# Optimization experiments

Hardware: AMD Instinct MI355X
Metric: run time of the kernel (lower is better)

Reference implementation:

```python
import jax, jax.numpy as jnp
import numpy as np

N_NODES = 100000
IN_CH = 256
HIDDEN = 256
N_EDGES = 500000


def setup_inputs() -> dict:
    key = jax.random.key(0)
    k_emb, k_ei, k_w1, k_w2 = jax.random.split(key, 4)
    embeddings = jax.random.normal(k_emb, (N_NODES, IN_CH), dtype=jnp.float32)
    edge_index = jax.random.randint(k_ei, (2, N_EDGES), 0, N_NODES, dtype=jnp.int64)
    # Linear(in*2, hidden) and Linear(hidden, 1) weights (stored input-major for x @ W)
    s1 = 1.0 / np.sqrt(2 * IN_CH)
    s2 = 1.0 / np.sqrt(HIDDEN)
    W1 = jax.random.uniform(k_w1, (2 * IN_CH, HIDDEN), dtype=jnp.float32, minval=-s1, maxval=s1)
    b1 = jnp.zeros((HIDDEN,), dtype=jnp.float32)
    W2 = jax.random.uniform(k_w2, (HIDDEN, 1), dtype=jnp.float32, minval=-s2, maxval=s2)
    b2 = jnp.zeros((1,), dtype=jnp.float32)
    return {"embeddings": embeddings, "edge_index": edge_index,
            "W1": W1, "b1": b1, "W2": W2, "b2": b2}


def reference(embeddings, edge_index, W1, b1, W2, b2):
    src, dst = edge_index[0], edge_index[1]
    # gather [E, in] twice, concat -> [E, 2*in]
    feats = jnp.concatenate([embeddings[src], embeddings[dst]], axis=-1)
    h = jax.nn.relu(feats @ W1 + b1)          # [E, hidden]
    scores = h @ W2 + b2                      # [E, 1]
    return scores.reshape(-1)
```

## Files before the change

### kernel.cpp

```cpp
#include <hip/hip_runtime.h>

#define NN   100000
#define EE   500000
#define MPAD 100096

using bf16x8 = __attribute__((ext_vector_type(8))) short;
using f32x4  = __attribute__((ext_vector_type(4))) float;
using u16x8  = __attribute__((ext_vector_type(8))) unsigned short;

__device__ __forceinline__ unsigned short f2bf(float f) {
  unsigned int x = __builtin_bit_cast(unsigned int, f);
  x += 0x7fffu + ((x >> 16) & 1u);
  return (unsigned short)(x >> 16);
}
__device__ __forceinline__ float bf2f(unsigned short u) {
  unsigned int x = ((unsigned int)u) << 16;
  return __builtin_bit_cast(float, x);
}

__global__ void wprep_kernel(const float* __restrict__ W1, unsigned short* __restrict__ WT) {
  int id = blockIdx.x * blockDim.x + threadIdx.x;
  if (id >= 512 * 32) return;
  int j  = id >> 5;
  int cg = id & 31;
  int jc = j & 255;
  int kb = (cg << 3) + ((j >= 256) ? 256 : 0);
  u16x8 v;
#pragma unroll
  for (int t = 0; t < 8; ++t)
    v[t] = f2bf(W1[(size_t)(kb + t) * 256 + jc]);
  *reinterpret_cast<u16x8*>(WT + (size_t)j * 256 + (cg << 3)) = v;
}

__global__ __launch_bounds__(512) void gemm_pq(const float* __restrict__ emb,
                                               const unsigned short* __restrict__ WT,
                                               const float* __restrict__ b1,
                                               unsigned short* __restrict__ R) {
  __shared__ unsigned short ldsA[2][128 * 32];
  __shared__ unsigned short ldsB[2][256 * 32];

  const int t    = threadIdx.x;
  const int lane = t & 63;
  const int wave = t >> 6;
  const int wrow = wave >> 2;
  const int wcol = wave & 3;
  const int m0   = (int)(blockIdx.x >> 1) * 128;
  const int n0   = (int)(blockIdx.x & 1) * 256;

  const int arow = t >> 2, ac = t & 3;
  const bool aOk = (m0 + arow) < NN;
  const float* aSrc = emb + (size_t)(m0 + arow) * 256 + (ac << 3);
  const int aW = arow * 32 + ((ac ^ ((arow >> 1) & 3)) << 3);

  const int brow = t >> 1, bh = t & 1;
  const unsigned short* bSrc = WT + (size_t)(n0 + brow) * 256 + (bh << 4);
  const int f_b = (brow >> 1) & 3;
  const int bW0 = brow * 32 + ((((bh << 1) | 0) ^ f_b) << 3);
  const int bW1 = brow * 32 + ((((bh << 1) | 1) ^ f_b) << 3);

  const int fr = lane & 15, fq = lane >> 4;
  int aoff[4], boff[4];
#pragma unroll
  for (int m = 0; m < 4; ++m) {
    int r = wrow * 64 + 16 * m + fr;
    aoff[m] = r * 32 + ((fq ^ ((r >> 1) & 3)) << 3);
  }
#pragma unroll
  for (int n = 0; n < 4; ++n) {
    int r = wcol * 64 + 16 * n + fr;
    boff[n] = r * 32 + ((fq ^ ((r >> 1) & 3)) << 3);
  }

  f32x4 acc[4][4] = {};

  {
    float4 a0, a1;
    if (aOk) { a0 = *(const float4*)aSrc; a1 = *(const float4*)(aSrc + 4); }
    else     { a0 = make_float4(0.f, 0.f, 0.f, 0.f); a1 = a0; }
    u16x8 b0 = *(const u16x8*)bSrc;
    u16x8 b1v = *(const u16x8*)(bSrc + 8);
    u16x8 aw;
    aw[0] = f2bf(a0.x); aw[1] = f2bf(a0.y); aw[2] = f2bf(a0.z); aw[3] = f2bf(a0.w);
    aw[4] = f2bf(a1.x); aw[5] = f2bf(a1.y); aw[6] = f2bf(a1.z); aw[7] = f2bf(a1.w);
    *(u16x8*)&ldsA[0][aW]  = aw;
    *(u16x8*)&ldsB[0][bW0] = b0;
    *(u16x8*)&ldsB[0][bW1] = b1v;
  }
  __syncthreads();

#pragma unroll
  for (int ks = 0; ks < 8; ++ks) {
    const int p = ks & 1;
    float4 na0, na1; u16x8 nb0, nb1;
    if (ks < 7) {
      const float* as = aSrc + ((ks + 1) << 5);
      if (aOk) { na0 = *(const float4*)as; na1 = *(const float4*)(as + 4); }
      else     { na0 = make_float4(0.f, 0.f, 0.f, 0.f); na1 = na0; }
      const unsigned short* bs = bSrc + ((ks + 1) << 5);
      nb0 = *(const u16x8*)bs;
      nb1 = *(const u16x8*)(bs + 8);
    }
    bf16x8 av[4], bv[4];
#pragma unroll
    for (int m = 0; m < 4; ++m) av[m] = *(const bf16x8*)&ldsA[p][aoff[m]];
#pragma unroll
    for (int n = 0; n < 4; ++n) bv[n] = *(const bf16x8*)&ldsB[p][boff[n]];
#pragma unroll
    for (int m = 0; m < 4; ++m)
#pragma unroll
      for (int n = 0; n < 4; ++n)
        acc[m][n] = __builtin_amdgcn_mfma_f32_16x16x32_bf16(av[m], bv[n], acc[m][n], 0, 0, 0);
    if (ks < 7) {
      u16x8 aw;
      aw[0] = f2bf(na0.x); aw[1] = f2bf(na0.y); aw[2] = f2bf(na0.z); aw[3] = f2bf(na0.w);
      aw[4] = f2bf(na1.x); aw[5] = f2bf(na1.y); aw[6] = f2bf(na1.z); aw[7] = f2bf(na1.w);
      *(u16x8*)&ldsA[p ^ 1][aW]  = aw;
      *(u16x8*)&ldsB[p ^ 1][bW0] = nb0;
      *(u16x8*)&ldsB[p ^ 1][bW1] = nb1;
    }
    __syncthreads();
  }

  float bn[4];
#pragma unroll
  for (int n = 0; n < 4; ++n) {
    const int c = n0 + wcol * 64 + 16 * n + fr;
    bn[n] = (c < 256) ? b1[c] : 0.f;
  }
#pragma unroll
  for (int m = 0; m < 4; ++m) {
    const int r0 = m0 + wrow * 64 + 16 * m + (fq << 2);
#pragma unroll
    for (int n = 0; n < 4; ++n) {
      const int c = n0 + wcol * 64 + 16 * n + fr;
#pragma unroll
      for (int i = 0; i < 4; ++i)
        R[(size_t)(r0 + i) * 512 + c] = f2bf(acc[m][n][i] + bn[n]);
    }
  }
}

__global__ __launch_bounds__(256) void edge_kernel(const int* __restrict__ idx,
                                                   const unsigned short* __restrict__ R,
                                                   const float* __restrict__ W2,
                                                   const float* __restrict__ b2,
                                                   float* __restrict__ out) {
  const int lane  = threadIdx.x & 63;
  const int half  = lane >> 5;
  const int l     = lane & 31;
  const int gwave = (int)((blockIdx.x * blockDim.x + threadIdx.x) >> 6);
  const int nwave = (int)((gridDim.x * blockDim.x) >> 6);
  const float4 w0 = *(const float4*)(W2 + (l << 3));
  const float4 w1 = *(const float4*)(W2 + (l << 3) + 4);
  const float bias = b2[0];

  for (int c = gwave; c < (EE / 8); c += nwave) {
    const int e0 = c << 3;
    int s[4], d[4];
#pragma unroll
    for (int u = 0; u < 4; ++u) {
      s[u] = idx[e0 + (u << 1) + half];
      d[u] = idx[EE + e0 + (u << 1) + half];
    }
    u16x8 ga[4], gb[4];
#pragma unroll
    for (int u = 0; u < 4; ++u) {
      ga[u] = *(const u16x8*)(R + (size_t)s[u] * 512 + (l << 3));
      gb[u] = *(const u16x8*)(R + (size_t)d[u] * 512 + 256 + (l << 3));
    }
#pragma unroll
    for (int u = 0; u < 4; ++u) {
      float acc;
      acc  = fmaxf(bf2f((unsigned short)ga[u][0]) + bf2f((unsigned short)gb[u][0]), 0.f) * w0.x;
      acc += fmaxf(bf2f((unsigned short)ga[u][1]) + bf2f((unsigned short)gb[u][1]), 0.f) * w0.y;
      acc += fmaxf(bf2f((unsigned short)ga[u][2]) + bf2f((unsigned short)gb[u][2]), 0.f) * w0.z;
      acc += fmaxf(bf2f((unsigned short)ga[u][3]) + bf2f((unsigned short)gb[u][3]), 0.f) * w0.w;
      acc += fmaxf(bf2f((unsigned short)ga[u][4]) + bf2f((unsigned short)gb[u][4]), 0.f) * w1.x;
      acc += fmaxf(bf2f((unsigned short)ga[u][5]) + bf2f((unsigned short)gb[u][5]), 0.f) * w1.y;
      acc += fmaxf(bf2f((unsigned short)ga[u][6]) + bf2f((unsigned short)gb[u][6]), 0.f) * w1.z;
      acc += fmaxf(bf2f((unsigned short)ga[u][7]) + bf2f((unsigned short)gb[u][7]), 0.f) * w1.w;
#pragma unroll
      for (int off = 16; off > 0; off >>= 1) acc += __shfl_xor(acc, off, 64);
      if (l == 0) out[e0 + (u << 1) + half] = acc + bias;
    }
  }
}

__global__ __launch_bounds__(256) void fallback_kernel(const float* __restrict__ emb,
                                                       const int* __restrict__ idx,
                                                       const float* __restrict__ W1,
                                                       const float* __restrict__ b1,
                                                       const float* __restrict__ W2,
                                                       const float* __restrict__ b2,
                                                       float* __restrict__ out) {
  __shared__ float feats[512];
  __shared__ float red[256];
  const int t = threadIdx.x;
  for (int e = blockIdx.x; e < EE; e += gridDim.x) {
    __syncthreads();
    const int s = idx[e], d = idx[EE + e];
    feats[t]       = emb[(size_t)s * 256 + t];
    feats[256 + t] = emb[(size_t)d * 256 + t];
    __syncthreads();
    float h = b1[t];
    for (int k = 0; k < 512; ++k) h += feats[k] * W1[k * 256 + t];
    red[t] = fmaxf(h, 0.f) * W2[t];
    __syncthreads();
    for (int off = 128; off > 0; off >>= 1) {
      if (t < off) red[t] += red[t + off];
      __syncthreads();
    }
    if (t == 0) out[e] = red[0] + b2[0];
  }
}

extern "C" void kernel_launch(void* const* d_in, const int* in_sizes, int n_in,
                              void* d_out, int out_size, void* d_ws, size_t ws_size,
                              hipStream_t stream) {
  const float* emb = (const float*)d_in[0];
  const int*   idx = (const int*)d_in[1];
  const float* W1  = (const float*)d_in[2];
  const float* b1  = (const float*)d_in[3];
  const float* W2  = (const float*)d_in[4];
  const float* b2  = (const float*)d_in[5];
  float* out = (float*)d_out;

  const size_t wt_elems = (size_t)512 * 256;
  const size_t r_elems  = (size_t)MPAD * 512;
  const size_t need = (wt_elems + r_elems) * sizeof(unsigned short);

  if (ws_size < need) {
    fallback_kernel<<<4096, 256, 0, stream>>>(emb, idx, W1, b1, W2, b2, out);
    return;
  }

  unsigned short* WT = (unsigned short*)d_ws;
  unsigned short* R  = WT + wt_elems;

  wprep_kernel<<<64, 256, 0, stream>>>(W1, WT);
  gemm_pq<<<782 * 2, 512, 0, stream>>>(emb, WT, b1, R);
  edge_kernel<<<2048, 256, 0, stream>>>(idx, R, W2, b2, out);
}
```

Before: 151.8 us.

## Shrink GEMM tile to 64 rows and read W1 fragments directly from global

The node-projection GEMM now uses 64-row tiles with 256-thread blocks, giving twice as many blocks. B fragments are loaded straight from global/L2 into registers instead of being staged through LDS. The K loop goes from 8 steps of 32 to 4 steps of 64 with double-buffered A, which halves the number of barriers. In exchange, B gets less reuse and global loads sit on the MFMA critical path, since B is not prefetched.

```diff
diff --git a/kernel.cpp b/kernel.cpp
--- a/kernel.cpp
+++ b/kernel.cpp
@@ -32,112 +32,116 @@
   *reinterpret_cast<u16x8*>(WT + (size_t)j * 256 + (cg << 3)) = v;
 }
 
-__global__ __launch_bounds__(512) void gemm_pq(const float* __restrict__ emb,
+__global__ __launch_bounds__(256) void gemm_pq(const float* __restrict__ emb,
                                                const unsigned short* __restrict__ WT,
                                                const float* __restrict__ b1,
                                                unsigned short* __restrict__ R) {
-  __shared__ unsigned short ldsA[2][128 * 32];
-  __shared__ unsigned short ldsB[2][256 * 32];
+  __shared__ unsigned short ldsA[2][2][64 * 32];
 
   const int t    = threadIdx.x;
   const int lane = t & 63;
   const int wave = t >> 6;
-  const int wrow = wave >> 2;
-  const int wcol = wave & 3;
-  const int m0   = (int)(blockIdx.x >> 1) * 128;
+  const int m0   = (int)(blockIdx.x >> 1) * 64;
   const int n0   = (int)(blockIdx.x & 1) * 256;
 
-  const int arow = t >> 2, ac = t & 3;
-  const bool aOk = (m0 + arow) < NN;
-  const float* aSrc = emb + (size_t)(m0 + arow) * 256 + (ac << 3);
-  const int aW = arow * 32 + ((ac ^ ((arow >> 1) & 3)) << 3);
-
-  const int brow = t >> 1, bh = t & 1;
-  const unsigned short* bSrc = WT + (size_t)(n0 + brow) * 256 + (bh << 4);
-  const int f_b = (brow >> 1) & 3;
-  const int bW0 = brow * 32 + ((((bh << 1) | 0) ^ f_b) << 3);
-  const int bW1 = brow * 32 + ((((bh << 1) | 1) ^ f_b) << 3);
+  const int a_r = t >> 2, a_j = t & 3;
+  const bool aOk = (m0 + a_r) < NN;
+  const float* aSrc = emb + (size_t)(m0 + a_r) * 256 + (a_j << 4);
+  const int a_s  = a_j >> 1;
+  const int fA   = (a_r >> 1) & 3;
+  const int aW0  = a_r * 32 + ((((a_j & 1) << 1) | 0) ^ fA) * 8;
+  const int aW1  = a_r * 32 + ((((a_j & 1) << 1) | 1) ^ fA) * 8;
 
   const int fr = lane & 15, fq = lane >> 4;
-  int aoff[4], boff[4];
+  const int fS = (fr >> 1) & 3;
+  int aoff[4];
+#pragma unroll
+  for (int m = 0; m < 4; ++m)
+    aoff[m] = (16 * m + fr) * 32 + ((fq ^ fS) << 3);
+
+  const unsigned short* bRow[4];
+#pragma unroll
+  for (int n = 0; n < 4; ++n)
+    bRow[n] = WT + (size_t)(n0 + wave * 64 + 16 * n + fr) * 256 + (fq << 3);
+
+  f32x4 acc[4][4] = {};
+  float4 pA[4];
+
+#define LOADA(kb)                                                              \
+  do {                                                                         \
+    if (aOk) {                                                                 \
+      pA[0] = *(const float4*)(aSrc + (kb));                                   \
+      pA[1] = *(const float4*)(aSrc + (kb) + 4);                               \
+      pA[2] = *(const float4*)(aSrc + (kb) + 8);                               \
+      pA[3] = *(const float4*)(aSrc + (kb) + 12);                              \
+    } else {                                                                   \
+      pA[0] = pA[1] = pA[2] = pA[3] = make_float4(0.f, 0.f, 0.f, 0.f);         \
+    }                                                                          \
+  } while (0)
+
+#define WRITEA(buf)                                                            \
+  do {                                                                         \
+    u16x8 w0, w1;                                                              \
+    w0[0] = f2bf(pA[0].x); w0[1] = f2bf(pA[0].y);                              \
+    w0[2] = f2bf(pA[0].z); w0[3] = f2bf(pA[0].w);                              \
+    w0[4] = f2bf(pA[1].x); w0[5] = f2bf(pA[1].y);                              \
+    w0[6] = f2bf(pA[1].z); w0[7] = f2bf(pA[1].w);                              \
+    w1[0] = f2bf(pA[2].x); w1[1] = f2bf(pA[2].y);                              \
+    w1[2] = f2bf(pA[2].z); w1[3] = f2bf(pA[2].w);                              \
+    w1[4] = f2bf(pA[3].x); w1[5] = f2bf(pA[3].y);                              \
+    w1[6] = f2bf(pA[3].z); w1[7] = f2bf(pA[3].w);                              \
+    *(u16x8*)&ldsA[(buf)][a_s][aW0] = w0;                                      \
+    *(u16x8*)&ldsA[(buf)][a_s][aW1] = w1;                                      \
+  } while (0)
+
+  LOADA(0);
+  WRITEA(0);
+  LOADA(64);
+  __syncthreads();
+
+#pragma unroll
+  for (int ks = 0; ks < 4; ++ks) {
+    const int p = ks & 1;
+#pragma unroll
+    for (int s = 0; s < 2; ++s) {
+      bf16x8 av[4], bv[4];
+#pragma unroll
+      for (int m = 0; m < 4; ++m) av[m] = *(const bf16x8*)&ldsA[p][s][aoff[m]];
+#pragma unroll
+      for (int n = 0; n < 4; ++n)
+        bv[n] = *(const bf16x8*)(bRow[n] + (ks << 6) + (s << 5));
+#pragma unroll
+      for (int m = 0; m < 4; ++m)
+#pragma unroll
+        for (int n = 0; n < 4; ++n)
+          acc[m][n] = __builtin_amdgcn_mfma_f32_16x16x32_bf16(av[m], bv[n], acc[m][n], 0, 0, 0);
+    }
+    if (ks < 3) {
+      WRITEA(p ^ 1);
+      if (ks < 2) LOADA((ks + 2) << 6);
+      __syncthreads();
+    }
+  }
+
+  float bn[4];
+#pragma unroll
+  for (int n = 0; n < 4; ++n) {
+    const int c = n0 + wave * 64 + 16 * n + fr;
+    bn[n] = (c < 256) ? b1[c] : 0.f;
+  }
 #pragma unroll
   for (int m = 0; m < 4; ++m) {
-    int r = wrow * 64 + 16 * m + fr;
-    aoff[m] = r * 32 + ((fq ^ ((r >> 1) & 3)) << 3);
-  }
-#pragma unroll
-  for (int n = 0; n < 4; ++n) {
-    int r = wcol * 64 + 16 * n + fr;
-    boff[n] = r * 32 + ((fq ^ ((r >> 1) & 3)) << 3);
-  }
-
-  f32x4 acc[4][4] = {};
-
-  {
-    float4 a0, a1;
-    if (aOk) { a0 = *(const float4*)aSrc; a1 = *(const float4*)(aSrc + 4); }
-    else     { a0 = make_float4(0.f, 0.f, 0.f, 0.f); a1 = a0; }
-    u16x8 b0 = *(const u16x8*)bSrc;
-    u16x8 b1v = *(const u16x8*)(bSrc + 8);
-    u16x8 aw;
-    aw[0] = f2bf(a0.x); aw[1] = f2bf(a0.y); aw[2] = f2bf(a0.z); aw[3] = f2bf(a0.w);
-    aw[4] = f2bf(a1.x); aw[5] = f2bf(a1.y); aw[6] = f2bf(a1.z); aw[7] = f2bf(a1.w);
-    *(u16x8*)&ldsA[0][aW]  = aw;
-    *(u16x8*)&ldsB[0][bW0] = b0;
-    *(u16x8*)&ldsB[0][bW1] = b1v;
-  }
-  __syncthreads();
-
-#pragma unroll
-  for (int ks = 0; ks < 8; ++ks) {
-    const int p = ks & 1;
-    float4 na0, na1; u16x8 nb0, nb1;
-    if (ks < 7) {
-      const float* as = aSrc + ((ks + 1) << 5);
-      if (aOk) { na0 = *(const float4*)as; na1 = *(const float4*)(as + 4); }
-      else     { na0 = make_float4(0.f, 0.f, 0.f, 0.f); na1 = na0; }
-      const unsigned short* bs = bSrc + ((ks + 1) << 5);
-      nb0 = *(const u16x8*)bs;
-      nb1 = *(const u16x8*)(bs + 8);
-    }
-    bf16x8 av[4], bv[4];
-#pragma unroll
-    for (int m = 0; m < 4; ++m) av[m] = *(const bf16x8*)&ldsA[p][aoff[m]];
-#pragma unroll
-    for (int n = 0; n < 4; ++n) bv[n] = *(const bf16x8*)&ldsB[p][boff[n]];
-#pragma unroll
-    for (int m = 0; m < 4; ++m)
-#pragma unroll
-      for (int n = 0; n < 4; ++n)
-        acc[m][n] = __builtin_amdgcn_mfma_f32_16x16x32_bf16(av[m], bv[n], acc[m][n], 0, 0, 0);
-    if (ks < 7) {
-      u16x8 aw;
-      aw[0] = f2bf(na0.x); aw[1] = f2bf(na0.y); aw[2] = f2bf(na0.z); aw[3] = f2bf(na0.w);
-      aw[4] = f2bf(na1.x); aw[5] = f2bf(na1.y); aw[6] = f2bf(na1.z); aw[7] = f2bf(na1.w);
-      *(u16x8*)&ldsA[p ^ 1][aW]  = aw;
-      *(u16x8*)&ldsB[p ^ 1][bW0] = nb0;
-      *(u16x8*)&ldsB[p ^ 1][bW1] = nb1;
-    }
-    __syncthreads();
-  }
-
-  float bn[4];
-#pragma unroll
-  for (int n = 0; n < 4; ++n) {
-    const int c = n0 + wcol * 64 + 16 * n + fr;
-    bn[n] = (c < 256) ? b1[c] : 0.f;
-  }
-#pragma unroll
-  for (int m = 0; m < 4; ++m) {
-    const int r0 = m0 + wrow * 64 + 16 * m + (fq << 2);
+    const int r0 = m0 + 16 * m + (fq << 2);
 #pragma unroll
     for (int n = 0; n < 4; ++n) {
-      const int c = n0 + wcol * 64 + 16 * n + fr;
+      const int c = n0 + wave * 64 + 16 * n + fr;
 #pragma unroll
       for (int i = 0; i < 4; ++i)
         R[(size_t)(r0 + i) * 512 + c] = f2bf(acc[m][n][i] + bn[n]);
     }
   }
+#undef LOADA
+#undef WRITEA
 }
 
 __global__ __launch_bounds__(256) void edge_kernel(const int* __restrict__ idx,
@@ -238,6 +242,6 @@
   unsigned short* R  = WT + wt_elems;
 
   wprep_kernel<<<64, 256, 0, stream>>>(W1, WT);
-  gemm_pq<<<782 * 2, 512, 0, stream>>>(emb, WT, b1, R);
+  gemm_pq<<<(MPAD / 64) * 2, 256, 0, stream>>>(emb, WT, b1, R);
   edge_kernel<<<2048, 256, 0, stream>>>(idx, R, W2, b2, out);
 }
```

Measured after the change: 163.0 us. +7.4%, slower.

## Retile node GEMM to 128x128 blocks with direct global-to-LDS weight loads

Applied to the files above, without the earlier changes.

The node-level GEMM moves from 512-thread blocks with 128x256 tiles to 256-thread blocks with 128x128 tiles at an occupancy hint of 3. The weight tile is now loaded straight into LDS with global_load_lds, and A loads are prefetched two stages ahead in registers. Block IDs are remapped across 8 groups for locality, and the final barrier is dropped. The aim is to overlap more memory latency and raise occupancy, at the cost of reading each embedding row four times instead of twice. Out-of-range rows are clamped rather than zeroed, and the LDS layout now depends on the swizzled global_load_lds addressing being correct.

```diff
diff --git a/kernel.cpp b/kernel.cpp
--- a/kernel.cpp
+++ b/kernel.cpp
@@ -1,4 +1,5 @@
 #include <hip/hip_runtime.h>
+#include <hip/hip_bf16.h>
 
 #define NN   100000
 #define EE   500000
@@ -16,6 +17,13 @@
 __device__ __forceinline__ float bf2f(unsigned short u) {
   unsigned int x = ((unsigned int)u) << 16;
   return __builtin_bit_cast(float, x);
+}
+__device__ __forceinline__ unsigned short f2bh(float f) {
+  return __builtin_bit_cast(unsigned short, __float2bfloat16(f));
+}
+__device__ __forceinline__ void glds16(const void* g, const void* l) {
+  __builtin_amdgcn_global_load_lds((const __attribute__((address_space(1))) void*)g,
+                                   (__attribute__((address_space(3))) void*)l, 16, 0, 0);
 }
 
 __global__ void wprep_kernel(const float* __restrict__ W1, unsigned short* __restrict__ WT) {
@@ -32,73 +40,97 @@
   *reinterpret_cast<u16x8*>(WT + (size_t)j * 256 + (cg << 3)) = v;
 }
 
-__global__ __launch_bounds__(512) void gemm_pq(const float* __restrict__ emb,
-                                               const unsigned short* __restrict__ WT,
-                                               const float* __restrict__ b1,
-                                               unsigned short* __restrict__ R) {
+__global__ __launch_bounds__(256, 3) void gemm_pq(const float* __restrict__ emb,
+                                                  const unsigned short* __restrict__ WT,
+                                                  const float* __restrict__ b1,
+                                                  unsigned short* __restrict__ R) {
   __shared__ unsigned short ldsA[2][128 * 32];
-  __shared__ unsigned short ldsB[2][256 * 32];
+  __shared__ unsigned short ldsB[2][128 * 32];
 
   const int t    = threadIdx.x;
   const int lane = t & 63;
   const int wave = t >> 6;
-  const int wrow = wave >> 2;
-  const int wcol = wave & 3;
-  const int m0   = (int)(blockIdx.x >> 1) * 128;
-  const int n0   = (int)(blockIdx.x & 1) * 256;
-
-  const int arow = t >> 2, ac = t & 3;
-  const bool aOk = (m0 + arow) < NN;
-  const float* aSrc = emb + (size_t)(m0 + arow) * 256 + (ac << 3);
-  const int aW = arow * 32 + ((ac ^ ((arow >> 1) & 3)) << 3);
-
-  const int brow = t >> 1, bh = t & 1;
-  const unsigned short* bSrc = WT + (size_t)(n0 + brow) * 256 + (bh << 4);
-  const int f_b = (brow >> 1) & 3;
-  const int bW0 = brow * 32 + ((((bh << 1) | 0) ^ f_b) << 3);
-  const int bW1 = brow * 32 + ((((bh << 1) | 1) ^ f_b) << 3);
+  const int wrow = wave >> 1, wcol = wave & 1;
+  const int bid = (int)blockIdx.x;
+  const int lid = (bid & 7) * 391 + (bid >> 3);
+  const int m0 = (lid >> 2) * 128;
+  const int n0 = (lid & 3) * 128;
+
+  const int a_r = t >> 1, a_h = t & 1;
+  int arow_g = m0 + a_r; if (arow_g >= NN) arow_g = NN - 1;
+  const float* aSrc = emb + (size_t)arow_g * 256 + (a_h << 4);
+  const int a_s  = (a_r >> 1) & 3;
+  const int aW0  = a_r * 32 + ((((a_h << 1) | 0) ^ a_s) << 3);
+  const int aW1  = a_r * 32 + ((((a_h << 1) | 1) ^ a_s) << 3);
+
+  size_t bOff[2]; int bLds[2];
+#pragma unroll
+  for (int i = 0; i < 2; ++i) {
+    const int r  = wave * 32 + i * 16 + (lane >> 2);
+    const int qp = lane & 3;
+    const int g  = qp ^ ((r >> 1) & 3);
+    bOff[i] = (size_t)(n0 + r) * 256 + (g << 3);
+    bLds[i] = (wave * 32 + i * 16) * 32;
+  }
 
   const int fr = lane & 15, fq = lane >> 4;
   int aoff[4], boff[4];
 #pragma unroll
   for (int m = 0; m < 4; ++m) {
-    int r = wrow * 64 + 16 * m + fr;
+    const int r = wrow * 64 + 16 * m + fr;
     aoff[m] = r * 32 + ((fq ^ ((r >> 1) & 3)) << 3);
   }
 #pragma unroll
   for (int n = 0; n < 4; ++n) {
-    int r = wcol * 64 + 16 * n + fr;
+    const int r = wcol * 64 + 16 * n + fr;
     boff[n] = r * 32 + ((fq ^ ((r >> 1) & 3)) << 3);
   }
 
   f32x4 acc[4][4] = {};
-
-  {
-    float4 a0, a1;
-    if (aOk) { a0 = *(const float4*)aSrc; a1 = *(const float4*)(aSrc + 4); }
-    else     { a0 = make_float4(0.f, 0.f, 0.f, 0.f); a1 = a0; }
-    u16x8 b0 = *(const u16x8*)bSrc;
-    u16x8 b1v = *(const u16x8*)(bSrc + 8);
-    u16x8 aw;
-    aw[0] = f2bf(a0.x); aw[1] = f2bf(a0.y); aw[2] = f2bf(a0.z); aw[3] = f2bf(a0.w);
-    aw[4] = f2bf(a1.x); aw[5] = f2bf(a1.y); aw[6] = f2bf(a1.z); aw[7] = f2bf(a1.w);
-    *(u16x8*)&ldsA[0][aW]  = aw;
-    *(u16x8*)&ldsB[0][bW0] = b0;
-    *(u16x8*)&ldsB[0][bW1] = b1v;
-  }
+  float4 pA[4];
+
+#define ALOAD(kb)                                                              \
+  do {                                                                         \
+    pA[0] = *(const float4*)(aSrc + (kb));                                     \
+    pA[1] = *(const float4*)(aSrc + (kb) + 4);                                 \
+    pA[2] = *(const float4*)(aSrc + (kb) + 8);                                 \
+    pA[3] = *(const float4*)(aSrc + (kb) + 12);                                \
+  } while (0)
+
+#define AWRITE(buf)                                                            \
+  do {                                                                         \
+    u16x8 w0, w1;                                                              \
+    w0[0] = f2bh(pA[0].x); w0[1] = f2bh(pA[0].y);                              \
+    w0[2] = f2bh(pA[0].z); w0[3] = f2bh(pA[0].w);                              \
+    w0[4] = f2bh(pA[1].x); w0[5] = f2bh(pA[1].y);                              \
+    w0[6] = f2bh(pA[1].z); w0[7] = f2bh(pA[1].w);                              \
+    w1[0] = f2bh(pA[2].x); w1[1] = f2bh(pA[2].y);                              \
+    w1[2] = f2bh(pA[2].z); w1[3] = f2bh(pA[2].w);                              \
+    w1[4] = f2bh(pA[3].x); w1[5] = f2bh(pA[3].y);                              \
+    w1[6] = f2bh(pA[3].z); w1[7] = f2bh(pA[3].w);                              \
+    *(u16x8*)&ldsA[(buf)][aW0] = w0;                                           \
+    *(u16x8*)&ldsA[(buf)][aW1] = w1;                                           \
+  } while (0)
+
+#define BGLDS(buf, kb)                                                         \
+  do {                                                                         \
+    glds16(WT + bOff[0] + (kb), &ldsB[(buf)][bLds[0]]);                        \
+    glds16(WT + bOff[1] + (kb), &ldsB[(buf)][bLds[1]]);                        \
+  } while (0)
+
+  ALOAD(0);
+  AWRITE(0);
+  BGLDS(0, 0);
+  ALOAD(32);
   __syncthreads();
 
 #pragma unroll
   for (int ks = 0; ks < 8; ++ks) {
     const int p = ks & 1;
-    float4 na0, na1; u16x8 nb0, nb1;
     if (ks < 7) {
-      const float* as = aSrc + ((ks + 1) << 5);
-      if (aOk) { na0 = *(const float4*)as; na1 = *(const float4*)(as + 4); }
-      else     { na0 = make_float4(0.f, 0.f, 0.f, 0.f); na1 = na0; }
-      const unsigned short* bs = bSrc + ((ks + 1) << 5);
-      nb0 = *(const u16x8*)bs;
-      nb1 = *(const u16x8*)(bs + 8);
+      BGLDS(p ^ 1, (ks + 1) * 32);
+      AWRITE(p ^ 1);
+      if (ks < 6) ALOAD((ks + 2) * 32);
     }
     bf16x8 av[4], bv[4];
 #pragma unroll
@@ -110,15 +142,7 @@
 #pragma unroll
       for (int n = 0; n < 4; ++n)
         acc[m][n] = __builtin_amdgcn_mfma_f32_16x16x32_bf16(av[m], bv[n], acc[m][n], 0, 0, 0);
-    if (ks < 7) {
-      u16x8 aw;
-      aw[0] = f2bf(na0.x); aw[1] = f2bf(na0.y); aw[2] = f2bf(na0.z); aw[3] = f2bf(na0.w);
-      aw[4] = f2bf(na1.x); aw[5] = f2bf(na1.y); aw[6] = f2bf(na1.z); aw[7] = f2bf(na1.w);
-      *(u16x8*)&ldsA[p ^ 1][aW]  = aw;
-      *(u16x8*)&ldsB[p ^ 1][bW0] = nb0;
-      *(u16x8*)&ldsB[p ^ 1][bW1] = nb1;
-    }
-    __syncthreads();
+    if (ks < 7) __syncthreads();
   }
 
   float bn[4];
@@ -138,6 +162,9 @@
         R[(size_t)(r0 + i) * 512 + c] = f2bf(acc[m][n][i] + bn[n]);
     }
   }
+#undef ALOAD
+#undef AWRITE
+#undef BGLDS
 }
 
 __global__ __launch_bounds__(256) void edge_kernel(const int* __restrict__ idx,
@@ -238,6 +265,6 @@
   unsigned short* R  = WT + wt_elems;
 
   wprep_kernel<<<64, 256, 0, stream>>>(W1, WT);
-  gemm_pq<<<782 * 2, 512, 0, stream>>>(emb, WT, b1, R);
+  gemm_pq<<<(MPAD / 128) * 4, 256, 0, stream>>>(emb, WT, b1, R);
   edge_kernel<<<2048, 256, 0, stream>>>(idx, R, W2, b2, out);
 }
```

Result: faster. 137.2 us (-9.6%).
